# Kernel tuning notes

Hardware: AMD Instinct MI355X
Metric: run time of the kernel (lower is better)

## Reference

```python
import jax, jax.numpy as jnp
import numpy as np

E = 1024
H = 16
D = E // H  # 64
S = 2048
B = 4


def setup_inputs() -> dict:
    key = jax.random.key(0)
    ks = jax.random.split(key, 9)
    scale = 1.0 / np.sqrt(E)
    inp = {"x": jax.random.normal(ks[0], (S, B, E), dtype=jnp.float32)}
    for i, name in enumerate(["q", "k", "v", "o"]):
        inp[f"W{name}"] = jax.random.uniform(ks[1 + 2 * i], (E, E), dtype=jnp.float32, minval=-scale, maxval=scale)
        inp[f"b{name}"] = jax.random.uniform(ks[2 + 2 * i], (E,), dtype=jnp.float32, minval=-scale, maxval=scale)
    return inp


def reference(x, Wq, bq, Wk, bk, Wv, bv, Wo, bo):
    s, b, e = x.shape
    # linear projections (torch Linear: x @ W.T + b), split into heads
    q = (x @ Wq.T + bq).reshape(s, b, H, D)
    k = (x @ Wk.T + bk).reshape(s, b, H, D)
    v = (x @ Wv.T + bv).reshape(s, b, H, D)
    # naive O(S^2) attention, scores: [S, B, H, S]
    scores = jnp.einsum('sbhd,tbhd->sbht', q, k) / np.sqrt(D).astype(np.float32)
    attn = jax.nn.softmax(scores, axis=3)
    # dropout p=0.0 (eval) -> identity
    out = jnp.einsum('sbht,tbhd->sbhd', attn, v).reshape(s, b, e)
    return out @ Wo.T + bo
```

## Files before the change

kernel.cpp:

```cpp
#include <hip/hip_runtime.h>
#include <hip/hip_bf16.h>

#define S_LEN 2048
#define BATCH 4
#define EMB   1024
#define NH    16
#define HD    64
#define NROW  8192

#define QSCALE 0.18033688011112043f

typedef __bf16 bf16x8 __attribute__((ext_vector_type(8)));
typedef float  f32x4  __attribute__((ext_vector_type(4)));

typedef __attribute__((address_space(3))) void lds_void;
typedef const __attribute__((address_space(1))) void gbl_void;
#define GLOAD_LDS16(g, l) __builtin_amdgcn_global_load_lds((gbl_void*)(g), (lds_void*)(l), 16, 0, 0)
#define MFMA16(a, b, c) __builtin_amdgcn_mfma_f32_16x16x32_bf16((a), (b), (c), 0, 0, 0)

#if __has_builtin(__builtin_amdgcn_exp2f)
#define EXP2(x) __builtin_amdgcn_exp2f(x)
#else
#define EXP2(x) __expf((x) * 0.6931471805599453f)
#endif

__global__ void cvt_all_kernel(const float* __restrict__ x,
                               const float* __restrict__ wq, const float* __restrict__ wk,
                               const float* __restrict__ wv, const float* __restrict__ wo,
                               __bf16* __restrict__ xb,
                               __bf16* __restrict__ qb, __bf16* __restrict__ kb,
                               __bf16* __restrict__ vb, __bf16* __restrict__ ob) {
    const int bid = blockIdx.x;
    const float* src;
    __bf16* dst;
    int i;
    if (bid < 8192) {
        src = x; dst = xb; i = bid * 256 + threadIdx.x;
    } else {
        const int w = (bid - 8192) >> 10;
        src = w == 0 ? wq : (w == 1 ? wk : (w == 2 ? wv : wo));
        dst = w == 0 ? qb : (w == 1 ? kb : (w == 2 ? vb : ob));
        i = ((bid - 8192) & 1023) * 256 + threadIdx.x;
    }
    float4 v = ((const float4*)src)[i];
    union { __bf16 h[4]; short4 s4; } u;
    u.h[0] = (__bf16)v.x; u.h[1] = (__bf16)v.y;
    u.h[2] = (__bf16)v.z; u.h[3] = (__bf16)v.w;
    ((short4*)dst)[i] = u.s4;
}

__global__ __launch_bounds__(256) void gemm_qkv_kernel(
    const __bf16* __restrict__ A,
    const __bf16* __restrict__ W0, const __bf16* __restrict__ W1,
    const __bf16* __restrict__ W2,
    const float* __restrict__ bi0, const float* __restrict__ bi1,
    const float* __restrict__ bi2,
    __bf16* __restrict__ Qo, __bf16* __restrict__ Ko, __bf16* __restrict__ Vo)
{
    __shared__ __align__(16) char SMEM[49152];
    __bf16* Asb = (__bf16*)SMEM;
    __bf16* Bsb = (__bf16*)(SMEM + 24576);

    const int flat = blockIdx.x;
    const int xcd = flat & 7, slot = flat >> 3;
    const int nB = slot >> 3;
    const int mB = (xcd << 3) | (slot & 7);
    const int which = nB >> 3;
    const __bf16* W = which == 0 ? W0 : (which == 1 ? W1 : W2);
    const float* bias = which == 0 ? bi0 : (which == 1 ? bi1 : bi2);
    __bf16* outb = which == 0 ? Qo : (which == 1 ? Ko : Vo);
    const int m0 = mB * 128;
    const int n0 = (nB & 7) * 128;

    const int lane = threadIdx.x & 63;
    const int wave = threadIdx.x >> 6;
    const int l15 = lane & 15;
    const int quad = lane >> 4;
    const int wm = (wave >> 1) * 64;
    const int wn = (wave & 1) * 64;

    const int c0 = wave * 128 + lane;
    const int c1 = c0 + 64;
    const int ar0 = c0 >> 2, ak0 = (((c0 & 3) ^ ((c0 >> 3) & 3))) * 8;
    const int ar1 = c1 >> 2, ak1 = (((c1 & 3) ^ ((c1 >> 3) & 3))) * 8;

    const __bf16* Ag = A + (size_t)m0 * EMB;
    const __bf16* Wg = W + (size_t)n0 * EMB;

    f32x4 acc[4][4];
#pragma unroll
    for (int i = 0; i < 4; ++i)
#pragma unroll
        for (int j = 0; j < 4; ++j) acc[i][j] = (f32x4){0.f, 0.f, 0.f, 0.f};

    auto stage = [&](int t, int buf) {
        const int kk = t * 32;
        GLOAD_LDS16(Ag + (size_t)ar0 * EMB + kk + ak0, Asb + buf * 4096 + wave * 1024);
        GLOAD_LDS16(Ag + (size_t)ar1 * EMB + kk + ak1, Asb + buf * 4096 + wave * 1024 + 512);
        GLOAD_LDS16(Wg + (size_t)ar0 * EMB + kk + ak0, Bsb + buf * 4096 + wave * 1024);
        GLOAD_LDS16(Wg + (size_t)ar1 * EMB + kk + ak1, Bsb + buf * 4096 + wave * 1024 + 512);
    };
    stage(0, 0);
    stage(1, 1);

    const int xr = (l15 >> 1) & 3;
    int bt = 0;
    for (int t = 0; t < 32; ++t) {
        if (t < 31) asm volatile("s_waitcnt vmcnt(4)" ::: "memory");
        else        asm volatile("s_waitcnt vmcnt(0)" ::: "memory");
        __builtin_amdgcn_s_barrier();
        if (t + 2 < 32) {
            int wb = bt + 2; if (wb >= 3) wb -= 3;
            stage(t + 2, wb);
        }
        bf16x8 af[4], bfr[4];
#pragma unroll
        for (int tt = 0; tt < 4; ++tt) {
            af[tt]  = *(const bf16x8*)(Asb + bt * 4096 + (wm + tt * 16 + l15) * 32 + ((quad ^ xr) << 3));
            bfr[tt] = *(const bf16x8*)(Bsb + bt * 4096 + (wn + tt * 16 + l15) * 32 + ((quad ^ xr) << 3));
        }
#pragma unroll
        for (int i = 0; i < 4; ++i)
#pragma unroll
            for (int j = 0; j < 4; ++j)
                acc[i][j] = MFMA16(af[i], bfr[j], acc[i][j]);
        if (++bt == 3) bt = 0;
    }

    __syncthreads();
    __bf16* epi = (__bf16*)SMEM + wave * 2304;
    float bv[4];
#pragma unroll
    for (int j = 0; j < 4; ++j) bv[j] = bias[n0 + wn + j * 16 + l15];
    const int hh = (n0 + wn) >> 6;

    if (which != 2) {
#pragma unroll
        for (int p = 0; p < 2; ++p) {
#pragma unroll
            for (int ih = 0; ih < 2; ++ih) {
                const int i = 2 * p + ih;
#pragma unroll
                for (int j = 0; j < 4; ++j)
#pragma unroll
                    for (int r = 0; r < 4; ++r) {
                        float v = acc[i][j][r] + bv[j];
                        if (which == 0) v *= QSCALE;
                        epi[(ih * 16 + quad * 4 + r) * 72 + j * 16 + l15] = (__bf16)v;
                    }
            }
#pragma unroll
            for (int ii = 0; ii < 4; ++ii) {
                const int rl = ii * 8 + (lane >> 3);
                bf16x8 row = *(const bf16x8*)(epi + rl * 72 + (lane & 7) * 8);
                const int m = m0 + wm + p * 32 + rl;
                const int b = m & 3, s = m >> 2;
                *(bf16x8*)(outb + ((size_t)(b * NH + hh) * S_LEN + s) * HD
                           + (lane & 7) * 8) = row;
            }
        }
    } else {
        const int sb = (m0 + wm) >> 2;
#pragma unroll
        for (int p = 0; p < 2; ++p) {
#pragma unroll
            for (int jh = 0; jh < 2; ++jh) {
                const int j = 2 * p + jh;
#pragma unroll
                for (int i = 0; i < 4; ++i)
#pragma unroll
                    for (int r = 0; r < 4; ++r) {
                        float v = acc[i][j][r] + bv[j];
                        epi[(jh * 16 + l15) * 72 + r * 16 + i * 4 + quad] = (__bf16)v;
                    }
            }
#pragma unroll
            for (int ii = 0; ii < 4; ++ii) {
                const int q = lane >> 1;
                bf16x8 row = *(const bf16x8*)(epi + q * 72 + ii * 16 + (lane & 1) * 8);
                const int d = p * 32 + q;
                *(bf16x8*)(outb + ((size_t)(ii * NH + hh) * HD + d) * S_LEN
                           + sb + (lane & 1) * 8) = row;
            }
        }
    }
}

__global__ __launch_bounds__(256) void gemm_out_kernel(
    const __bf16* __restrict__ A, const __bf16* __restrict__ W,
    const float* __restrict__ bias, float* __restrict__ outf)
{
    __shared__ __bf16 As[3][128 * 32];
    __shared__ __bf16 Bs[3][128 * 32];
    const int flat = blockIdx.x;
    const int xcd = flat & 7, slot = flat >> 3;
    const int nB = slot >> 3;
    const int mB = (xcd << 3) | (slot & 7);
    const int m0 = mB * 128;
    const int n0 = nB * 128;

    const int lane = threadIdx.x & 63;
    const int wave = threadIdx.x >> 6;
    const int l15 = lane & 15;
    const int quad = lane >> 4;
    const int wm = (wave >> 1) * 64;
    const int wn = (wave & 1) * 64;

    const int c0 = wave * 128 + lane;
    const int c1 = c0 + 64;
    const int ar0 = c0 >> 2, ak0 = (((c0 & 3) ^ ((c0 >> 3) & 3))) * 8;
    const int ar1 = c1 >> 2, ak1 = (((c1 & 3) ^ ((c1 >> 3) & 3))) * 8;

    const __bf16* Ag = A + (size_t)m0 * EMB;
    const __bf16* Wg = W + (size_t)n0 * EMB;

    f32x4 acc[4][4];
#pragma unroll
    for (int i = 0; i < 4; ++i)
#pragma unroll
        for (int j = 0; j < 4; ++j) acc[i][j] = (f32x4){0.f, 0.f, 0.f, 0.f};

    auto stage = [&](int t, int buf) {
        const int kk = t * 32;
        GLOAD_LDS16(Ag + (size_t)ar0 * EMB + kk + ak0, &As[buf][wave * 1024]);
        GLOAD_LDS16(Ag + (size_t)ar1 * EMB + kk + ak1, &As[buf][wave * 1024 + 512]);
        GLOAD_LDS16(Wg + (size_t)ar0 * EMB + kk + ak0, &Bs[buf][wave * 1024]);
        GLOAD_LDS16(Wg + (size_t)ar1 * EMB + kk + ak1, &Bs[buf][wave * 1024 + 512]);
    };
    stage(0, 0);
    stage(1, 1);

    const int xr = (l15 >> 1) & 3;
    int bt = 0;
    for (int t = 0; t < 32; ++t) {
        if (t < 31) asm volatile("s_waitcnt vmcnt(4)" ::: "memory");
        else        asm volatile("s_waitcnt vmcnt(0)" ::: "memory");
        __builtin_amdgcn_s_barrier();
        if (t + 2 < 32) {
            int wb = bt + 2; if (wb >= 3) wb -= 3;
            stage(t + 2, wb);
        }
        bf16x8 af[4], bfr[4];
#pragma unroll
        for (int tt = 0; tt < 4; ++tt) {
            af[tt]  = *(const bf16x8*)(&As[bt][0] + (wm + tt * 16 + l15) * 32 + ((quad ^ xr) << 3));
            bfr[tt] = *(const bf16x8*)(&Bs[bt][0] + (wn + tt * 16 + l15) * 32 + ((quad ^ xr) << 3));
        }
#pragma unroll
        for (int i = 0; i < 4; ++i)
#pragma unroll
            for (int j = 0; j < 4; ++j)
                acc[i][j] = MFMA16(af[i], bfr[j], acc[i][j]);
        if (++bt == 3) bt = 0;
    }

#pragma unroll
    for (int j = 0; j < 4; ++j) {
        const int col = n0 + wn + j * 16 + l15;
        const float bv = bias[col];
#pragma unroll
        for (int i = 0; i < 4; ++i)
#pragma unroll
            for (int r = 0; r < 4; ++r) {
                const int m = m0 + wm + i * 16 + quad * 4 + r;
                outf[(size_t)m * EMB + col] = acc[i][j][r] + bv;
            }
    }
}

__global__ __launch_bounds__(256, 3) void attn_kernel(
    const __bf16* __restrict__ Q, const __bf16* __restrict__ Kp,
    const __bf16* __restrict__ Vt, __bf16* __restrict__ Ao)
{
    __shared__ __align__(16) __bf16 Ks[3][32 * 64];
    __shared__ __align__(16) __bf16 Vs[4][32 * 64];
    __shared__ __align__(16) __bf16 Ps[4][2][32 * 40];

    const int tid = threadIdx.x;
    const int lane = tid & 63;
    const int wave = tid >> 6;
    const int l15 = lane & 15;
    const int quad = lane >> 4;

    const int flat = blockIdx.y * gridDim.x + blockIdx.x;
    const int nf = (flat & 7) * 128 + (flat >> 3);
    const int bh = nf >> 4;
    const int b = bh >> 4, h = bh & 15;
    const int qw = (nf & 15) * 128 + wave * 32;

    const __bf16* Qb = Q  + (size_t)bh * S_LEN * HD;
    const __bf16* Kb = Kp + (size_t)bh * S_LEN * HD;
    const __bf16* Vb = Vt + (size_t)bh * HD * S_LEN;

    const int kr = tid >> 3;
    const int ks = (((tid & 7) ^ ((tid >> 4) & 7))) * 8;
    const int vr = tid >> 2;
    const int vs = (((tid & 3) ^ ((tid >> 3) & 3))) * 8;

    bf16x8 qf[2][2];
#pragma unroll
    for (int mi = 0; mi < 2; ++mi)
#pragma unroll
        for (int kc = 0; kc < 2; ++kc)
            qf[mi][kc] = *(const bf16x8*)(Qb + (size_t)(qw + mi * 16 + l15) * HD
                                          + kc * 32 + quad * 8);

    bf16x8 ones;
#pragma unroll
    for (int i = 0; i < 8; ++i) ones[i] = (__bf16)1.0f;

    f32x4 acco[2][4], accl[2];
#pragma unroll
    for (int mi = 0; mi < 2; ++mi) {
        accl[mi] = (f32x4){0.f, 0.f, 0.f, 0.f};
#pragma unroll
        for (int nt = 0; nt < 4; ++nt) acco[mi][nt] = (f32x4){0.f, 0.f, 0.f, 0.f};
    }

    auto stageKV = [&](int t) {
        const int t0 = t * 32;
        GLOAD_LDS16(Kb + (size_t)(t0 + kr) * HD + ks, &Ks[t % 3][wave * 512]);
        GLOAD_LDS16(Vb + (size_t)vr * S_LEN + t0 + vs, &Vs[t & 3][wave * 512]);
    };

    auto qk_exp = [&](int it) {
        const __bf16* Kt = &Ks[it % 3][0];
        __bf16* Pw = &Ps[wave][it & 1][0];
        bf16x8 kf[2][2];
#pragma unroll
        for (int p = 0; p < 2; ++p) {
            const int r = 2 * l15 + p;
            const int x = l15 & 7;
#pragma unroll
            for (int kc = 0; kc < 2; ++kc)
                kf[p][kc] = *(const bf16x8*)(Kt + r * 64 + (((kc * 4 + quad) ^ x) << 3));
        }
#pragma unroll
        for (int mi = 0; mi < 2; ++mi) {
            f32x4 se = {0.f, 0.f, 0.f, 0.f}, so = {0.f, 0.f, 0.f, 0.f};
            se = MFMA16(qf[mi][0], kf[0][0], se);
            se = MFMA16(qf[mi][1], kf[0][1], se);
            so = MFMA16(qf[mi][0], kf[1][0], so);
            so = MFMA16(qf[mi][1], kf[1][1], so);
#pragma unroll
            for (int r = 0; r < 4; ++r) {
                float pe = EXP2(se[r]);
                float po = EXP2(so[r]);
                union { __bf16 hh[2]; unsigned u; } pk;
                pk.hh[0] = (__bf16)pe;
                pk.hh[1] = (__bf16)po;
                *(unsigned*)(Pw + (mi * 16 + quad * 4 + r) * 40 + 2 * l15) = pk.u;
            }
        }
    };

    auto pv = [&](int it) {
        const __bf16* Vl = &Vs[it & 3][0];
        const __bf16* Pw = &Ps[wave][it & 1][0];
        bf16x8 pf[2];
#pragma unroll
        for (int mi = 0; mi < 2; ++mi) {
            pf[mi] = *(const bf16x8*)(Pw + (mi * 16 + l15) * 40 + quad * 8);
            accl[mi] = MFMA16(pf[mi], ones, accl[mi]);
        }
#pragma unroll
        for (int nt = 0; nt < 4; ++nt) {
            const int rv = nt * 16 + l15;
            const int xv = (l15 >> 1) & 3;
            bf16x8 vf = *(const bf16x8*)(Vl + rv * 32 + (((quad ^ xv)) << 3));
#pragma unroll
            for (int mi = 0; mi < 2; ++mi)
                acco[mi][nt] = MFMA16(pf[mi], vf, acco[mi][nt]);
        }
    };

    stageKV(0);
    stageKV(1);

    asm volatile("s_waitcnt vmcnt(2)" ::: "memory");
    __builtin_amdgcn_s_barrier();
    stageKV(2);
    qk_exp(0);

    for (int it = 1; it < S_LEN / 32; ++it) {
        if (it < S_LEN / 32 - 1) asm volatile("s_waitcnt vmcnt(2)" ::: "memory");
        else                     asm volatile("s_waitcnt vmcnt(0)" ::: "memory");
        __builtin_amdgcn_s_barrier();
        if (it + 2 < S_LEN / 32) stageKV(it + 2);
        pv(it - 1);
        qk_exp(it);
    }
    pv(S_LEN / 32 - 1);

#pragma unroll
    for (int mi = 0; mi < 2; ++mi)
#pragma unroll
        for (int r = 0; r < 4; ++r) {
            const float inv = 1.0f / accl[mi][r];
            const int srow = qw + mi * 16 + quad * 4 + r;
            const int n = srow * BATCH + b;
#pragma unroll
            for (int nt = 0; nt < 4; ++nt)
                Ao[(size_t)n * EMB + h * 64 + nt * 16 + l15] =
                    (__bf16)(acco[mi][nt][r] * inv);
        }
}

extern "C" void kernel_launch(void* const* d_in, const int* in_sizes, int n_in,
                              void* d_out, int out_size, void* d_ws, size_t ws_size,
                              hipStream_t stream) {
    const float* x  = (const float*)d_in[0];
    const float* Wq = (const float*)d_in[1];
    const float* bq = (const float*)d_in[2];
    const float* Wk = (const float*)d_in[3];
    const float* bk = (const float*)d_in[4];
    const float* Wv = (const float*)d_in[5];
    const float* bv = (const float*)d_in[6];
    const float* Wo = (const float*)d_in[7];
    const float* bo = (const float*)d_in[8];
    float* out = (float*)d_out;

    char* ws = (char*)d_ws;
    const size_t xbf_sz = (size_t)NROW * EMB * 2;
    const size_t wbf_sz = (size_t)EMB * EMB * 2;
    const size_t qkv_sz = (size_t)BATCH * NH * S_LEN * HD * 2;
    __bf16* x_bf  = (__bf16*)ws;  ws += xbf_sz;
    __bf16* Wq_bf = (__bf16*)ws;  ws += wbf_sz;
    __bf16* Wk_bf = (__bf16*)ws;  ws += wbf_sz;
    __bf16* Wv_bf = (__bf16*)ws;  ws += wbf_sz;
    __bf16* Wo_bf = (__bf16*)ws;  ws += wbf_sz;
    __bf16* Qb    = (__bf16*)ws;  ws += qkv_sz;
    __bf16* Kb    = (__bf16*)ws;  ws += qkv_sz;
    __bf16* Vtb   = (__bf16*)ws;  ws += qkv_sz;
    __bf16* Aob   = (__bf16*)ws;  ws += qkv_sz;

    cvt_all_kernel<<<8192 + 4 * 1024, 256, 0, stream>>>(
        x, Wq, Wk, Wv, Wo, x_bf, Wq_bf, Wk_bf, Wv_bf, Wo_bf);

    gemm_qkv_kernel<<<64 * 24, 256, 0, stream>>>(x_bf, Wq_bf, Wk_bf, Wv_bf,
                                                 bq, bk, bv, Qb, Kb, Vtb);
    dim3 ag(S_LEN / 128, BATCH * NH);
    attn_kernel<<<ag, 256, 0, stream>>>(Qb, Kb, Vtb, Aob);
    gemm_out_kernel<<<(NROW / 128) * (EMB / 128), 256, 0, stream>>>(Aob, Wo_bf, bo, out);
}
```

Measured before the change: 288.9 us.

## Double query rows per wave in attention and reorder QK/PV pipeline

Each wave now handles 64 query rows instead of 32, so a block covers 256 queries and the grid shrinks to 512 blocks. Each K/V tile loaded into LDS is therefore reused across twice as many queries. The loop is reordered to issue the QK MFMAs first, then the PV of the previous tile, then the exp and P write, so MFMA work can overlap the exp latency. V is staged one tile ahead in a 3-deep buffer, and P uses a single buffer per wave. The cost is higher register pressure: the occupancy hint of 3 is removed and the grid is smaller, which risks lower occupancy and a partial wave.

```diff
diff --git a/kernel.cpp b/kernel.cpp
--- a/kernel.cpp
+++ b/kernel.cpp
@@ -268,13 +268,13 @@
     }
 }
 
-__global__ __launch_bounds__(256, 3) void attn_kernel(
+__global__ __launch_bounds__(256) void attn_kernel(
     const __bf16* __restrict__ Q, const __bf16* __restrict__ Kp,
     const __bf16* __restrict__ Vt, __bf16* __restrict__ Ao)
 {
     __shared__ __align__(16) __bf16 Ks[3][32 * 64];
-    __shared__ __align__(16) __bf16 Vs[4][32 * 64];
-    __shared__ __align__(16) __bf16 Ps[4][2][32 * 40];
+    __shared__ __align__(16) __bf16 Vs[3][32 * 64];
+    __shared__ __align__(16) __bf16 Ps[4][64 * 40];
 
     const int tid = threadIdx.x;
     const int lane = tid & 63;
@@ -282,11 +282,11 @@
     const int l15 = lane & 15;
     const int quad = lane >> 4;
 
-    const int flat = blockIdx.y * gridDim.x + blockIdx.x;
-    const int nf = (flat & 7) * 128 + (flat >> 3);
-    const int bh = nf >> 4;
+    const int flat = blockIdx.x;
+    const int nf = (flat & 7) * 64 + (flat >> 3);
+    const int bh = nf >> 3;
     const int b = bh >> 4, h = bh & 15;
-    const int qw = (nf & 15) * 128 + wave * 32;
+    const int qw = (nf & 7) * 256 + wave * 64;
 
     const __bf16* Qb = Q  + (size_t)bh * S_LEN * HD;
     const __bf16* Kb = Kp + (size_t)bh * S_LEN * HD;
@@ -297,9 +297,9 @@
     const int vr = tid >> 2;
     const int vs = (((tid & 3) ^ ((tid >> 3) & 3))) * 8;
 
-    bf16x8 qf[2][2];
-#pragma unroll
-    for (int mi = 0; mi < 2; ++mi)
+    bf16x8 qf[4][2];
+#pragma unroll
+    for (int mi = 0; mi < 4; ++mi)
 #pragma unroll
         for (int kc = 0; kc < 2; ++kc)
             qf[mi][kc] = *(const bf16x8*)(Qb + (size_t)(qw + mi * 16 + l15) * HD
@@ -309,23 +309,25 @@
 #pragma unroll
     for (int i = 0; i < 8; ++i) ones[i] = (__bf16)1.0f;
 
-    f32x4 acco[2][4], accl[2];
-#pragma unroll
-    for (int mi = 0; mi < 2; ++mi) {
+    f32x4 acco[4][4], accl[4];
+#pragma unroll
+    for (int mi = 0; mi < 4; ++mi) {
         accl[mi] = (f32x4){0.f, 0.f, 0.f, 0.f};
 #pragma unroll
         for (int nt = 0; nt < 4; ++nt) acco[mi][nt] = (f32x4){0.f, 0.f, 0.f, 0.f};
     }
 
-    auto stageKV = [&](int t) {
-        const int t0 = t * 32;
-        GLOAD_LDS16(Kb + (size_t)(t0 + kr) * HD + ks, &Ks[t % 3][wave * 512]);
-        GLOAD_LDS16(Vb + (size_t)vr * S_LEN + t0 + vs, &Vs[t & 3][wave * 512]);
-    };
-
-    auto qk_exp = [&](int it) {
+    auto stageK = [&](int t) {
+        GLOAD_LDS16(Kb + (size_t)(t * 32 + kr) * HD + ks, &Ks[t % 3][wave * 512]);
+    };
+    auto stageV = [&](int t) {
+        GLOAD_LDS16(Vb + (size_t)vr * S_LEN + t * 32 + vs, &Vs[t % 3][wave * 512]);
+    };
+
+    __bf16* Pw = &Ps[wave][0];
+
+    auto qk = [&](int it, f32x4 (&se)[4], f32x4 (&so)[4]) {
         const __bf16* Kt = &Ks[it % 3][0];
-        __bf16* Pw = &Ps[wave][it & 1][0];
         bf16x8 kf[2][2];
 #pragma unroll
         for (int p = 0; p < 2; ++p) {
@@ -336,30 +338,35 @@
                 kf[p][kc] = *(const bf16x8*)(Kt + r * 64 + (((kc * 4 + quad) ^ x) << 3));
         }
 #pragma unroll
-        for (int mi = 0; mi < 2; ++mi) {
-            f32x4 se = {0.f, 0.f, 0.f, 0.f}, so = {0.f, 0.f, 0.f, 0.f};
-            se = MFMA16(qf[mi][0], kf[0][0], se);
-            se = MFMA16(qf[mi][1], kf[0][1], se);
-            so = MFMA16(qf[mi][0], kf[1][0], so);
-            so = MFMA16(qf[mi][1], kf[1][1], so);
+        for (int mi = 0; mi < 4; ++mi) {
+            se[mi] = (f32x4){0.f, 0.f, 0.f, 0.f};
+            so[mi] = (f32x4){0.f, 0.f, 0.f, 0.f};
+            se[mi] = MFMA16(qf[mi][0], kf[0][0], se[mi]);
+            se[mi] = MFMA16(qf[mi][1], kf[0][1], se[mi]);
+            so[mi] = MFMA16(qf[mi][0], kf[1][0], so[mi]);
+            so[mi] = MFMA16(qf[mi][1], kf[1][1], so[mi]);
+        }
+    };
+
+    auto sm_write = [&](f32x4 (&se)[4], f32x4 (&so)[4]) {
+#pragma unroll
+        for (int mi = 0; mi < 4; ++mi)
 #pragma unroll
             for (int r = 0; r < 4; ++r) {
-                float pe = EXP2(se[r]);
-                float po = EXP2(so[r]);
+                float pe = EXP2(se[mi][r]);
+                float po = EXP2(so[mi][r]);
                 union { __bf16 hh[2]; unsigned u; } pk;
                 pk.hh[0] = (__bf16)pe;
                 pk.hh[1] = (__bf16)po;
                 *(unsigned*)(Pw + (mi * 16 + quad * 4 + r) * 40 + 2 * l15) = pk.u;
             }
-        }
     };
 
     auto pv = [&](int it) {
-        const __bf16* Vl = &Vs[it & 3][0];
-        const __bf16* Pw = &Ps[wave][it & 1][0];
-        bf16x8 pf[2];
-#pragma unroll
-        for (int mi = 0; mi < 2; ++mi) {
+        const __bf16* Vl = &Vs[it % 3][0];
+        bf16x8 pf[4];
+#pragma unroll
+        for (int mi = 0; mi < 4; ++mi) {
             pf[mi] = *(const bf16x8*)(Pw + (mi * 16 + l15) * 40 + quad * 8);
             accl[mi] = MFMA16(pf[mi], ones, accl[mi]);
         }
@@ -369,31 +376,37 @@
             const int xv = (l15 >> 1) & 3;
             bf16x8 vf = *(const bf16x8*)(Vl + rv * 32 + (((quad ^ xv)) << 3));
 #pragma unroll
-            for (int mi = 0; mi < 2; ++mi)
+            for (int mi = 0; mi < 4; ++mi)
                 acco[mi][nt] = MFMA16(pf[mi], vf, acco[mi][nt]);
         }
     };
 
-    stageKV(0);
-    stageKV(1);
+    stageK(0); stageV(0); stageK(1);
 
     asm volatile("s_waitcnt vmcnt(2)" ::: "memory");
     __builtin_amdgcn_s_barrier();
-    stageKV(2);
-    qk_exp(0);
+    stageK(2); stageV(1);
+    {
+        f32x4 se[4], so[4];
+        qk(0, se, so);
+        sm_write(se, so);
+    }
 
     for (int it = 1; it < S_LEN / 32; ++it) {
         if (it < S_LEN / 32 - 1) asm volatile("s_waitcnt vmcnt(2)" ::: "memory");
         else                     asm volatile("s_waitcnt vmcnt(0)" ::: "memory");
         __builtin_amdgcn_s_barrier();
-        if (it + 2 < S_LEN / 32) stageKV(it + 2);
+        if (it + 2 < S_LEN / 32) stageK(it + 2);
+        if (it + 1 < S_LEN / 32) stageV(it + 1);
+        f32x4 se[4], so[4];
+        qk(it, se, so);
         pv(it - 1);
-        qk_exp(it);
+        sm_write(se, so);
     }
     pv(S_LEN / 32 - 1);
 
 #pragma unroll
-    for (int mi = 0; mi < 2; ++mi)
+    for (int mi = 0; mi < 4; ++mi)
 #pragma unroll
         for (int r = 0; r < 4; ++r) {
             const float inv = 1.0f / accl[mi][r];
@@ -439,7 +452,6 @@
 
     gemm_qkv_kernel<<<64 * 24, 256, 0, stream>>>(x_bf, Wq_bf, Wk_bf, Wv_bf,
                                                  bq, bk, bv, Qb, Kb, Vtb);
-    dim3 ag(S_LEN / 128, BATCH * NH);
-    attn_kernel<<<ag, 256, 0, stream>>>(Qb, Kb, Vtb, Aob);
+    attn_kernel<<<512, 256, 0, stream>>>(Qb, Kb, Vtb, Aob);
     gemm_out_kernel<<<(NROW / 128) * (EMB / 128), 256, 0, stream>>>(Aob, Wo_bf, bo, out);
 }
```

Measured after the change: 299.1 us. 1.04x slower.
